# Optimization experiments

Measured on AMD Instinct MI355X. Metric: run time of the kernel, lower is better.

## Reference

```python
import jax, jax.numpy as jnp
import numpy as np

B, H, N, D, M = 4, 16, 4096, 64, 64  # batch, heads, seq, dim_heads, nb_features


def setup_inputs() -> dict:
    key = jax.random.key(0)
    kq, kk, kv, kp = jax.random.split(key, 4)
    # positive-uniform q/k/projection keep the causal cumsum denominator > 0
    q = jax.random.uniform(kq, (B, H, N, D), dtype=jnp.float32)
    k = jax.random.uniform(kk, (B, H, N, D), dtype=jnp.float32)
    v = jax.random.normal(kv, (B, H, N, D), dtype=jnp.float32)
    projection = jax.random.uniform(kp, (M, D), dtype=jnp.float32)  # ortho_scaling=1 applied
    return {"q": q, "k": k, "v": v, "projection": projection}


def reference(q, k, v, projection):
    # feature map: project q, k into nb_features space  [B,H,N,M]
    qp = q @ projection.T
    kp = k @ projection.T
    # causal branch of FastAttention.forward (as written in the source):
    # denominator uses cumulative k features, numerator uses full context
    k_cumsum = jnp.cumsum(kp, axis=-2)                      # [B,H,N,M]
    D_inv = 1.0 / jnp.einsum('bhnm,bhnm->bhn', qp, k_cumsum)  # [B,H,N]
    context = jnp.einsum('bhnm,bhne->bhme', kp, v)          # [B,H,M,D]
    out = jnp.einsum('bhme,bhnm,bhn->bhne', context, qp, D_inv)  # [B,H,N,D]
    return out
```

## Files before the change

### kernel.cpp

```cpp
#include <hip/hip_runtime.h>

#define NN 4096
#define BHH 64

#define OFF_G  0
#define OFF_S  4096
#define OFF_T  (OFF_S + 64*4096)
#define OFF_GS (OFF_T + 64*4096)
#define OFF_PG (OFF_GS + 64*128*64)

__global__ void kA_gram(const float* __restrict__ P, float* __restrict__ G) {
    int i = blockIdx.x;
    int j = threadIdx.x;
    float acc = 0.f;
    for (int m = 0; m < 64; ++m)
        acc += P[m*64 + i] * P[m*64 + j];
    G[i*64 + j] = acc;
}

__launch_bounds__(256)
__global__ void kB(const float* __restrict__ k, const float* __restrict__ v,
                   const float* __restrict__ G, float* __restrict__ kg_out,
                   float* __restrict__ S, float* __restrict__ gs) {
    __shared__ __align__(16) float Gs[64*64];
    __shared__ __align__(16) float kt[32*68];
    __shared__ __align__(16) float vt[32*68];

    int t = threadIdx.x;
    int head = blockIdx.y, chunk = blockIdx.x;
    long base = ((long)head*NN + (long)chunk*256) * 64;

    float4*       Gs4 = (float4*)Gs;
    const float4* G4  = (const float4*)G;
#pragma unroll
    for (int i = 0; i < 4; ++i) Gs4[t + 256*i] = G4[t + 256*i];

    int dg = t >> 4, eg = t & 15;
    int rg = t >> 4, cg = t & 15;
    float accS[4][4] = {};

    float4* kt4 = (float4*)kt;
    float4* vt4 = (float4*)vt;

    for (int s = 0; s < 8; ++s) {
        __syncthreads();
        const float4* kgl = (const float4*)(k + base + (long)s*32*64);
        const float4* vgl = (const float4*)(v + base + (long)s*32*64);
#pragma unroll
        for (int i = 0; i < 2; ++i) {
            int f = t + 256*i;
            int r = f >> 4, c = f & 15;
            kt4[r*17 + c] = kgl[f];
            vt4[r*17 + c] = vgl[f];
        }
        __syncthreads();

#pragma unroll 4
        for (int r = 0; r < 32; ++r) {
            float4 kv = kt4[r*17 + dg];
            float4 vv = vt4[r*17 + eg];
            float ks[4] = {kv.x, kv.y, kv.z, kv.w};
            float vs[4] = {vv.x, vv.y, vv.z, vv.w};
#pragma unroll
            for (int i = 0; i < 4; ++i)
#pragma unroll
                for (int j = 0; j < 4; ++j)
                    accS[i][j] += ks[i]*vs[j];
        }

        float a[2][4] = {};
#pragma unroll
        for (int kq = 0; kq < 16; ++kq) {
            float4 ga0 = Gs4[(kq*4+0)*16 + cg];
            float4 ga1 = Gs4[(kq*4+1)*16 + cg];
            float4 ga2 = Gs4[(kq*4+2)*16 + cg];
            float4 ga3 = Gs4[(kq*4+3)*16 + cg];
            float4 ka = kt4[(rg*2+0)*17 + kq];
            float4 kb = kt4[(rg*2+1)*17 + kq];
            float gg[4][4] = {{ga0.x,ga0.y,ga0.z,ga0.w},{ga1.x,ga1.y,ga1.z,ga1.w},
                              {ga2.x,ga2.y,ga2.z,ga2.w},{ga3.x,ga3.y,ga3.z,ga3.w}};
            float kaa[4] = {ka.x,ka.y,ka.z,ka.w};
            float kbb[4] = {kb.x,kb.y,kb.z,kb.w};
#pragma unroll
            for (int u = 0; u < 4; ++u)
#pragma unroll
                for (int j = 0; j < 4; ++j) {
                    a[0][j] += kaa[u]*gg[u][j];
                    a[1][j] += kbb[u]*gg[u][j];
                }
        }
        float4* kgo = (float4*)(kg_out + base + (long)s*32*64);
        kgo[(rg*2+0)*16 + cg] = make_float4(a[0][0],a[0][1],a[0][2],a[0][3]);
        kgo[(rg*2+1)*16 + cg] = make_float4(a[1][0],a[1][1],a[1][2],a[1][3]);

        if (t < 64) {
            float gsum = 0.f;
#pragma unroll 8
            for (int r = 0; r < 32; ++r) gsum += kt[r*68 + t];
            gs[((long)head*128 + chunk*8 + s)*64 + t] = gsum;
        }
    }

#pragma unroll
    for (int i = 0; i < 4; ++i)
#pragma unroll
        for (int j = 0; j < 4; ++j)
            atomicAdd(&S[head*4096 + (dg*4+i)*64 + (eg*4+j)], accS[i][j]);
}

__launch_bounds__(256)
__global__ void kC(const float* __restrict__ G, const float* __restrict__ S,
                   float* __restrict__ T, const float* __restrict__ gs,
                   float* __restrict__ pg) {
    __shared__ float Gsp[64*65];
    __shared__ __align__(16) float Ss[64*64];
    __shared__ float kpre[128*65];

    int t = threadIdx.x;
    int head = blockIdx.x;

    for (int idx = t; idx < 4096; idx += 256)
        Gsp[(idx>>6)*65 + (idx&63)] = G[idx];
    const float4* S4  = (const float4*)(S + head*4096);
    float4*       Ss4 = (float4*)Ss;
#pragma unroll
    for (int i = 0; i < 4; ++i) Ss4[t + 256*i] = S4[t + 256*i];

    if (t < 64) {
        float run = 0.f;
        for (int g = 0; g < 128; ++g) {
            float x = gs[((long)head*128 + g)*64 + t];
            kpre[g*65 + t] = run;
            run += x;
        }
    }
    __syncthreads();

    {
        int ig = t >> 4, jg = t & 15;
        float acc[4][4] = {};
        for (int kk = 0; kk < 64; ++kk) {
            float4 sv = Ss4[kk*16 + jg];
            float svv[4] = {sv.x, sv.y, sv.z, sv.w};
            float gr[4];
#pragma unroll
            for (int i = 0; i < 4; ++i) gr[i] = Gsp[(ig*4+i)*65 + kk];
#pragma unroll
            for (int i = 0; i < 4; ++i)
#pragma unroll
                for (int j = 0; j < 4; ++j)
                    acc[i][j] += gr[i]*svv[j];
        }
        float4* T4 = (float4*)(T + head*4096);
#pragma unroll
        for (int i = 0; i < 4; ++i)
            T4[(ig*4+i)*16 + jg] = make_float4(acc[i][0],acc[i][1],acc[i][2],acc[i][3]);
    }

    {
        int g0 = (t >> 4) * 8, c0 = (t & 15) * 4;
        float acc[8][4] = {};
        for (int d = 0; d < 64; ++d) {
            float gr[4];
#pragma unroll
            for (int j = 0; j < 4; ++j) gr[j] = Gsp[d*65 + c0 + j];
#pragma unroll
            for (int i = 0; i < 8; ++i) {
                float kv = kpre[(g0+i)*65 + d];
#pragma unroll
                for (int j = 0; j < 4; ++j) acc[i][j] += kv*gr[j];
            }
        }
        float4* pg4 = (float4*)(pg + (long)head*128*64);
#pragma unroll
        for (int i = 0; i < 8; ++i)
            pg4[(g0+i)*16 + (t&15)] = make_float4(acc[i][0],acc[i][1],acc[i][2],acc[i][3]);
    }
}

__launch_bounds__(256)
__global__ void kD(const float* __restrict__ q, const float* __restrict__ kg,
                   const float* __restrict__ T, const float* __restrict__ pg,
                   float* __restrict__ out) {
    __shared__ __align__(16) float Ts[64*64];
    __shared__ float qs[4][32*65];
    __shared__ float dinvs[4][32];

    int t = threadIdx.x;
    int w = t >> 6, lane = t & 63;
    int head = blockIdx.y, tile = blockIdx.x;
    int g = tile*4 + w;
    long rowbase = (long)head*NN + (long)g*32;

    const float4* T4  = (const float4*)(T + head*4096);
    float4*       Ts4 = (float4*)Ts;
#pragma unroll
    for (int i = 0; i < 4; ++i) Ts4[t + 256*i] = T4[t + 256*i];

    float ckg = pg[((long)head*128 + g)*64 + lane];
#pragma unroll 4
    for (int r = 0; r < 32; ++r) {
        long off = (rowbase + r)*64 + lane;
        float qv  = q[off];
        float kgv = kg[off];
        ckg += kgv;
        float p = qv * ckg;
#pragma unroll
        for (int o = 32; o; o >>= 1) p += __shfl_xor(p, o, 64);
        qs[w][r*65 + lane] = qv;
        if (lane == 0) dinvs[w][r] = __builtin_amdgcn_rcpf(p);
    }
    __syncthreads();

    int rg = lane >> 3, cg = lane & 7;
    float acc[4][8] = {};
#pragma unroll 8
    for (int kk = 0; kk < 64; ++kk) {
        float4 t0 = Ts4[kk*16 + cg*2];
        float4 t1 = Ts4[kk*16 + cg*2 + 1];
        float tv[8] = {t0.x,t0.y,t0.z,t0.w,t1.x,t1.y,t1.z,t1.w};
#pragma unroll
        for (int i = 0; i < 4; ++i) {
            float qv = qs[w][(rg*4+i)*65 + kk];
#pragma unroll
            for (int j = 0; j < 8; ++j) acc[i][j] += qv*tv[j];
        }
    }
#pragma unroll
    for (int i = 0; i < 4; ++i) {
        float dv = dinvs[w][rg*4 + i];
        long o = (rowbase + rg*4 + i)*64 + cg*8;
        *(float4*)(out + o)     = make_float4(acc[i][0]*dv, acc[i][1]*dv, acc[i][2]*dv, acc[i][3]*dv);
        *(float4*)(out + o + 4) = make_float4(acc[i][4]*dv, acc[i][5]*dv, acc[i][6]*dv, acc[i][7]*dv);
    }
}

extern "C" void kernel_launch(void* const* d_in, const int* in_sizes, int n_in,
                              void* d_out, int out_size, void* d_ws, size_t ws_size,
                              hipStream_t stream) {
    (void)in_sizes; (void)n_in; (void)out_size; (void)ws_size;
    const float* q = (const float*)d_in[0];
    const float* k = (const float*)d_in[1];
    const float* v = (const float*)d_in[2];
    const float* P = (const float*)d_in[3];
    float* out = (float*)d_out;
    float* ws  = (float*)d_ws;

    float* G  = ws + OFF_G;
    float* S  = ws + OFF_S;
    float* T  = ws + OFF_T;
    float* gs = ws + OFF_GS;
    float* pg = ws + OFF_PG;

    hipMemsetAsync(S, 0, (size_t)64*4096*sizeof(float), stream);
    kA_gram<<<64, 64, 0, stream>>>(P, G);
    kB<<<dim3(16, 64), 256, 0, stream>>>(k, v, G, out, S, gs);
    kC<<<64, 256, 0, stream>>>(G, S, T, gs, pg);
    kD<<<dim3(32, 64), 256, 0, stream>>>(q, out, T, pg, out);
}
```

Before: 368.5 us.

## Restructure pipeline to apply Gram matrix to q in final kernel

Drops the per-row k·G product and the T=G·S precompute. The final kernel now forms q·G per tile, takes a running sum of raw k for the denominator, and multiplies the normalised qG by S directly. kB only accumulates kᵀv using an 8x8 register tile with a split-row reduction through shared memory, plus chunk sums of k. This removes writing and re-reading the kg intermediate through the output buffer, at the cost of more shared memory and extra compute in kD.

```diff
diff --git a/kernel.cpp b/kernel.cpp
--- a/kernel.cpp
+++ b/kernel.cpp
@@ -1,13 +1,11 @@
 #include <hip/hip_runtime.h>
 
 #define NN 4096
-#define BHH 64
-
-#define OFF_G  0
-#define OFF_S  4096
-#define OFF_T  (OFF_S + 64*4096)
-#define OFF_GS (OFF_T + 64*4096)
-#define OFF_PG (OFF_GS + 64*128*64)
+
+#define OFF_G   0
+#define OFF_S   4096
+#define OFF_GS  (OFF_S + 64*4096)
+#define OFF_KP  (OFF_GS + 64*128*64)
 
 __global__ void kA_gram(const float* __restrict__ P, float* __restrict__ G) {
     int i = blockIdx.x;
@@ -18,36 +16,29 @@
     G[i*64 + j] = acc;
 }
 
-__launch_bounds__(256)
+__launch_bounds__(256, 4)
 __global__ void kB(const float* __restrict__ k, const float* __restrict__ v,
-                   const float* __restrict__ G, float* __restrict__ kg_out,
                    float* __restrict__ S, float* __restrict__ gs) {
-    __shared__ __align__(16) float Gs[64*64];
-    __shared__ __align__(16) float kt[32*68];
-    __shared__ __align__(16) float vt[32*68];
+    __shared__ __align__(16) float kt[64*68];
+    __shared__ __align__(16) float vt[64*68];
 
     int t = threadIdx.x;
     int head = blockIdx.y, chunk = blockIdx.x;
     long base = ((long)head*NN + (long)chunk*256) * 64;
 
-    float4*       Gs4 = (float4*)Gs;
-    const float4* G4  = (const float4*)G;
-#pragma unroll
-    for (int i = 0; i < 4; ++i) Gs4[t + 256*i] = G4[t + 256*i];
-
-    int dg = t >> 4, eg = t & 15;
-    int rg = t >> 4, cg = t & 15;
-    float accS[4][4] = {};
+    int tg = t >> 6, l = t & 63;
+    int dg = l >> 3, eg = l & 7;
+    float acc[8][8] = {};
 
     float4* kt4 = (float4*)kt;
     float4* vt4 = (float4*)vt;
 
-    for (int s = 0; s < 8; ++s) {
+    for (int tile = 0; tile < 4; ++tile) {
         __syncthreads();
-        const float4* kgl = (const float4*)(k + base + (long)s*32*64);
-        const float4* vgl = (const float4*)(v + base + (long)s*32*64);
-#pragma unroll
-        for (int i = 0; i < 2; ++i) {
+        const float4* kgl = (const float4*)(k + base + (long)tile*64*64);
+        const float4* vgl = (const float4*)(v + base + (long)tile*64*64);
+#pragma unroll
+        for (int i = 0; i < 4; ++i) {
             int f = t + 256*i;
             int r = f >> 4, c = f & 15;
             kt4[r*17 + c] = kgl[f];
@@ -56,182 +47,188 @@
         __syncthreads();
 
 #pragma unroll 4
-        for (int r = 0; r < 32; ++r) {
-            float4 kv = kt4[r*17 + dg];
-            float4 vv = vt4[r*17 + eg];
-            float ks[4] = {kv.x, kv.y, kv.z, kv.w};
-            float vs[4] = {vv.x, vv.y, vv.z, vv.w};
-#pragma unroll
-            for (int i = 0; i < 4; ++i)
-#pragma unroll
-                for (int j = 0; j < 4; ++j)
-                    accS[i][j] += ks[i]*vs[j];
-        }
-
-        float a[2][4] = {};
-#pragma unroll
-        for (int kq = 0; kq < 16; ++kq) {
-            float4 ga0 = Gs4[(kq*4+0)*16 + cg];
-            float4 ga1 = Gs4[(kq*4+1)*16 + cg];
-            float4 ga2 = Gs4[(kq*4+2)*16 + cg];
-            float4 ga3 = Gs4[(kq*4+3)*16 + cg];
-            float4 ka = kt4[(rg*2+0)*17 + kq];
-            float4 kb = kt4[(rg*2+1)*17 + kq];
-            float gg[4][4] = {{ga0.x,ga0.y,ga0.z,ga0.w},{ga1.x,ga1.y,ga1.z,ga1.w},
-                              {ga2.x,ga2.y,ga2.z,ga2.w},{ga3.x,ga3.y,ga3.z,ga3.w}};
-            float kaa[4] = {ka.x,ka.y,ka.z,ka.w};
-            float kbb[4] = {kb.x,kb.y,kb.z,kb.w};
-#pragma unroll
-            for (int u = 0; u < 4; ++u)
-#pragma unroll
-                for (int j = 0; j < 4; ++j) {
-                    a[0][j] += kaa[u]*gg[u][j];
-                    a[1][j] += kbb[u]*gg[u][j];
-                }
-        }
-        float4* kgo = (float4*)(kg_out + base + (long)s*32*64);
-        kgo[(rg*2+0)*16 + cg] = make_float4(a[0][0],a[0][1],a[0][2],a[0][3]);
-        kgo[(rg*2+1)*16 + cg] = make_float4(a[1][0],a[1][1],a[1][2],a[1][3]);
-
-        if (t < 64) {
-            float gsum = 0.f;
+        for (int rr = 0; rr < 16; ++rr) {
+            int r = tg*16 + rr;
+            float4 ka = kt4[r*17 + dg*2];
+            float4 kb = kt4[r*17 + dg*2 + 1];
+            float4 va = vt4[r*17 + eg*2];
+            float4 vb = vt4[r*17 + eg*2 + 1];
+            float kk8[8] = {ka.x,ka.y,ka.z,ka.w,kb.x,kb.y,kb.z,kb.w};
+            float vv8[8] = {va.x,va.y,va.z,va.w,vb.x,vb.y,vb.z,vb.w};
+#pragma unroll
+            for (int i = 0; i < 8; ++i)
+#pragma unroll
+                for (int j = 0; j < 8; ++j)
+                    acc[i][j] += kk8[i]*vv8[j];
+        }
+
+        if (t < 128) {
+            int wv = t >> 6, m = t & 63;
+            float s = 0.f;
 #pragma unroll 8
-            for (int r = 0; r < 32; ++r) gsum += kt[r*68 + t];
-            gs[((long)head*128 + chunk*8 + s)*64 + t] = gsum;
-        }
-    }
-
-#pragma unroll
-    for (int i = 0; i < 4; ++i)
-#pragma unroll
-        for (int j = 0; j < 4; ++j)
-            atomicAdd(&S[head*4096 + (dg*4+i)*64 + (eg*4+j)], accS[i][j]);
+            for (int r2 = 0; r2 < 32; ++r2) s += kt[(wv*32 + r2)*68 + m];
+            gs[((long)head*128 + chunk*8 + tile*2 + wv)*64 + m] = s;
+        }
+    }
+
+    __syncthreads();
+    float* buf = (tg & 1) ? vt : kt;
+    if (tg < 2) {
+#pragma unroll
+        for (int x = 0; x < 64; ++x)
+            buf[l*68 + ((x + l) & 63)] = acc[x >> 3][x & 7];
+    }
+    __syncthreads();
+    if (tg >= 2) {
+#pragma unroll
+        for (int x = 0; x < 64; ++x)
+            buf[l*68 + ((x + l) & 63)] += acc[x >> 3][x & 7];
+    }
+    __syncthreads();
+    if (tg == 0) {
+#pragma unroll
+        for (int x = 0; x < 64; ++x) {
+            int xi = (x + l) & 63;
+            float vsum = kt[l*68 + xi] + vt[l*68 + xi];
+            int i = x >> 3, j = x & 7;
+            atomicAdd(&S[head*4096 + (dg*8 + i)*64 + eg*8 + j], vsum);
+        }
+    }
 }
 
 __launch_bounds__(256)
-__global__ void kC(const float* __restrict__ G, const float* __restrict__ S,
-                   float* __restrict__ T, const float* __restrict__ gs,
-                   float* __restrict__ pg) {
-    __shared__ float Gsp[64*65];
-    __shared__ __align__(16) float Ss[64*64];
-    __shared__ float kpre[128*65];
-
+__global__ void kC(const float* __restrict__ gs, float* __restrict__ kpre) {
+    __shared__ __align__(16) float gL[128*68];
     int t = threadIdx.x;
     int head = blockIdx.x;
 
-    for (int idx = t; idx < 4096; idx += 256)
-        Gsp[(idx>>6)*65 + (idx&63)] = G[idx];
-    const float4* S4  = (const float4*)(S + head*4096);
-    float4*       Ss4 = (float4*)Ss;
-#pragma unroll
-    for (int i = 0; i < 4; ++i) Ss4[t + 256*i] = S4[t + 256*i];
+    const float4* gs4 = (const float4*)(gs + (long)head*128*64);
+    float4* gL4 = (float4*)gL;
+#pragma unroll
+    for (int i = 0; i < 8; ++i) {
+        int f = t + 256*i;
+        int r = f >> 4, c = f & 15;
+        gL4[r*17 + c] = gs4[f];
+    }
+    __syncthreads();
 
     if (t < 64) {
         float run = 0.f;
         for (int g = 0; g < 128; ++g) {
-            float x = gs[((long)head*128 + g)*64 + t];
-            kpre[g*65 + t] = run;
-            run += x;
-        }
-    }
-    __syncthreads();
-
-    {
-        int ig = t >> 4, jg = t & 15;
-        float acc[4][4] = {};
-        for (int kk = 0; kk < 64; ++kk) {
-            float4 sv = Ss4[kk*16 + jg];
-            float svv[4] = {sv.x, sv.y, sv.z, sv.w};
-            float gr[4];
-#pragma unroll
-            for (int i = 0; i < 4; ++i) gr[i] = Gsp[(ig*4+i)*65 + kk];
-#pragma unroll
-            for (int i = 0; i < 4; ++i)
-#pragma unroll
-                for (int j = 0; j < 4; ++j)
-                    acc[i][j] += gr[i]*svv[j];
-        }
-        float4* T4 = (float4*)(T + head*4096);
-#pragma unroll
-        for (int i = 0; i < 4; ++i)
-            T4[(ig*4+i)*16 + jg] = make_float4(acc[i][0],acc[i][1],acc[i][2],acc[i][3]);
-    }
-
-    {
-        int g0 = (t >> 4) * 8, c0 = (t & 15) * 4;
-        float acc[8][4] = {};
-        for (int d = 0; d < 64; ++d) {
-            float gr[4];
-#pragma unroll
-            for (int j = 0; j < 4; ++j) gr[j] = Gsp[d*65 + c0 + j];
-#pragma unroll
-            for (int i = 0; i < 8; ++i) {
-                float kv = kpre[(g0+i)*65 + d];
-#pragma unroll
-                for (int j = 0; j < 4; ++j) acc[i][j] += kv*gr[j];
-            }
-        }
-        float4* pg4 = (float4*)(pg + (long)head*128*64);
-#pragma unroll
-        for (int i = 0; i < 8; ++i)
-            pg4[(g0+i)*16 + (t&15)] = make_float4(acc[i][0],acc[i][1],acc[i][2],acc[i][3]);
-    }
-}
-
-__launch_bounds__(256)
-__global__ void kD(const float* __restrict__ q, const float* __restrict__ kg,
-                   const float* __restrict__ T, const float* __restrict__ pg,
-                   float* __restrict__ out) {
-    __shared__ __align__(16) float Ts[64*64];
-    __shared__ float qs[4][32*65];
-    __shared__ float dinvs[4][32];
+            kpre[((long)head*128 + g)*64 + t] = run;
+            run += gL[g*68 + t];
+        }
+    }
+}
+
+__launch_bounds__(256, 2)
+__global__ void kD(const float* __restrict__ q, const float* __restrict__ k,
+                   const float* __restrict__ G, const float* __restrict__ S,
+                   const float* __restrict__ kpre, float* __restrict__ out) {
+    __shared__ __align__(16) float buf0[128*64];
+    __shared__ __align__(16) float qgs[128*64];
+    __shared__ __align__(16) float gsb[64*64];
 
     int t = threadIdx.x;
     int w = t >> 6, lane = t & 63;
     int head = blockIdx.y, tile = blockIdx.x;
-    int g = tile*4 + w;
-    long rowbase = (long)head*NN + (long)g*32;
-
-    const float4* T4  = (const float4*)(T + head*4096);
-    float4*       Ts4 = (float4*)Ts;
-#pragma unroll
-    for (int i = 0; i < 4; ++i) Ts4[t + 256*i] = T4[t + 256*i];
-
-    float ckg = pg[((long)head*128 + g)*64 + lane];
+    long rowbase = (long)head*NN + (long)tile*128;
+
+    int rg = t >> 3;
+    int cg = t & 7;
+    int lrg = (t >> 3) & 7;
+
+    float4* buf04 = (float4*)buf0;
+    float4* qgs4  = (float4*)qgs;
+    float4* gsb4  = (float4*)gsb;
+
+    const float4* qgl = (const float4*)(q + rowbase*64);
+#pragma unroll
+    for (int i = 0; i < 8; ++i) buf04[t + 256*i] = qgl[t + 256*i];
+    const float4* Ggl = (const float4*)G;
+#pragma unroll
+    for (int i = 0; i < 4; ++i) gsb4[t + 256*i] = Ggl[t + 256*i];
+    __syncthreads();
+
+    {
+        float a2[4][8] = {};
+        for (int kk0 = 0; kk0 < 64; ++kk0) {
+            int kk = (kk0 + 4*lrg) & 63;
+            float4 b0 = gsb4[kk*16 + cg*2];
+            float4 b1 = gsb4[kk*16 + cg*2 + 1];
+            float bb[8] = {b0.x,b0.y,b0.z,b0.w,b1.x,b1.y,b1.z,b1.w};
+#pragma unroll
+            for (int i = 0; i < 4; ++i) {
+                float av = buf0[(rg*4 + i)*64 + kk];
+#pragma unroll
+                for (int j = 0; j < 8; ++j) a2[i][j] += av*bb[j];
+            }
+        }
+#pragma unroll
+        for (int i = 0; i < 4; ++i) {
+            qgs4[(rg*4 + i)*16 + cg*2]     = make_float4(a2[i][0],a2[i][1],a2[i][2],a2[i][3]);
+            qgs4[(rg*4 + i)*16 + cg*2 + 1] = make_float4(a2[i][4],a2[i][5],a2[i][6],a2[i][7]);
+        }
+    }
+    __syncthreads();
+
+    const float4* kgl = (const float4*)(k + rowbase*64);
+#pragma unroll
+    for (int i = 0; i < 8; ++i) buf04[t + 256*i] = kgl[t + 256*i];
+    const float4* Sgl = (const float4*)(S + head*4096);
+#pragma unroll
+    for (int i = 0; i < 4; ++i) gsb4[t + 256*i] = Sgl[t + 256*i];
+    float pre = kpre[((long)head*128 + tile*4 + w)*64 + lane];
+    __syncthreads();
+
+    {
+        float c = pre;
 #pragma unroll 4
-    for (int r = 0; r < 32; ++r) {
-        long off = (rowbase + r)*64 + lane;
-        float qv  = q[off];
-        float kgv = kg[off];
-        ckg += kgv;
-        float p = qv * ckg;
-#pragma unroll
-        for (int o = 32; o; o >>= 1) p += __shfl_xor(p, o, 64);
-        qs[w][r*65 + lane] = qv;
-        if (lane == 0) dinvs[w][r] = __builtin_amdgcn_rcpf(p);
-    }
-    __syncthreads();
-
-    int rg = lane >> 3, cg = lane & 7;
-    float acc[4][8] = {};
+        for (int r = 0; r < 32; ++r) {
+            int idx = (w*32 + r)*64 + lane;
+            c += buf0[idx];
+            buf0[idx] = c;
+        }
+    }
+    __syncthreads();
+
+    if (t < 128) {
+        float d = 0.f;
 #pragma unroll 8
-    for (int kk = 0; kk < 64; ++kk) {
-        float4 t0 = Ts4[kk*16 + cg*2];
-        float4 t1 = Ts4[kk*16 + cg*2 + 1];
-        float tv[8] = {t0.x,t0.y,t0.z,t0.w,t1.x,t1.y,t1.z,t1.w};
+        for (int m0 = 0; m0 < 64; ++m0) {
+            int m = (m0 + t) & 63;
+            d += qgs[t*64 + m] * buf0[t*64 + m];
+        }
+        float dinv = __builtin_amdgcn_rcpf(d);
+#pragma unroll 8
+        for (int m0 = 0; m0 < 64; ++m0) {
+            int m = (m0 + t) & 63;
+            qgs[t*64 + m] *= dinv;
+        }
+    }
+    __syncthreads();
+
+    {
+        float o[4][8] = {};
+        for (int kk0 = 0; kk0 < 64; ++kk0) {
+            int kk = (kk0 + 4*lrg) & 63;
+            float4 b0 = gsb4[kk*16 + cg*2];
+            float4 b1 = gsb4[kk*16 + cg*2 + 1];
+            float bb[8] = {b0.x,b0.y,b0.z,b0.w,b1.x,b1.y,b1.z,b1.w};
+#pragma unroll
+            for (int i = 0; i < 4; ++i) {
+                float av = qgs[(rg*4 + i)*64 + kk];
+#pragma unroll
+                for (int j = 0; j < 8; ++j) o[i][j] += av*bb[j];
+            }
+        }
+        float4* out4 = (float4*)out;
 #pragma unroll
         for (int i = 0; i < 4; ++i) {
-            float qv = qs[w][(rg*4+i)*65 + kk];
-#pragma unroll
-            for (int j = 0; j < 8; ++j) acc[i][j] += qv*tv[j];
-        }
-    }
-#pragma unroll
-    for (int i = 0; i < 4; ++i) {
-        float dv = dinvs[w][rg*4 + i];
-        long o = (rowbase + rg*4 + i)*64 + cg*8;
-        *(float4*)(out + o)     = make_float4(acc[i][0]*dv, acc[i][1]*dv, acc[i][2]*dv, acc[i][3]*dv);
-        *(float4*)(out + o + 4) = make_float4(acc[i][4]*dv, acc[i][5]*dv, acc[i][6]*dv, acc[i][7]*dv);
+            long r = rowbase + rg*4 + i;
+            out4[r*16 + cg*2]     = make_float4(o[i][0],o[i][1],o[i][2],o[i][3]);
+            out4[r*16 + cg*2 + 1] = make_float4(o[i][4],o[i][5],o[i][6],o[i][7]);
+        }
     }
 }
 
@@ -246,15 +243,14 @@
     float* out = (float*)d_out;
     float* ws  = (float*)d_ws;
 
-    float* G  = ws + OFF_G;
-    float* S  = ws + OFF_S;
-    float* T  = ws + OFF_T;
-    float* gs = ws + OFF_GS;
-    float* pg = ws + OFF_PG;
+    float* G    = ws + OFF_G;
+    float* S    = ws + OFF_S;
+    float* gs   = ws + OFF_GS;
+    float* kpre = ws + OFF_KP;
 
     hipMemsetAsync(S, 0, (size_t)64*4096*sizeof(float), stream);
     kA_gram<<<64, 64, 0, stream>>>(P, G);
-    kB<<<dim3(16, 64), 256, 0, stream>>>(k, v, G, out, S, gs);
-    kC<<<64, 256, 0, stream>>>(G, S, T, gs, pg);
-    kD<<<dim3(32, 64), 256, 0, stream>>>(q, out, T, pg, out);
-}
+    kB<<<dim3(16, 64), 256, 0, stream>>>(k, v, S, gs);
+    kC<<<64, 256, 0, stream>>>(gs, kpre);
+    kD<<<dim3(32, 64), 256, 0, stream>>>(q, k, G, S, kpre, out);
+}
```

Measured after the change: 386.5 us. +4.9%, slower.
